# Kernel optimization log

Measured on AMD Instinct MI355X. Metric: run time of the kernel, lower is better.

The kernel has to match this reference:

```python
import jax, jax.numpy as jnp
import numpy as np

N_NODES = 50000
N_EDGES = 300000
D = 256


def setup_inputs() -> dict:
    key = jax.random.key(0)
    k1, k2, k3, k4, k5 = jax.random.split(key, 5)
    edge_feat = jax.random.normal(k1, (N_EDGES, D), dtype=jnp.float32)
    node_feat = jax.random.normal(k2, (N_NODES, D), dtype=jnp.float32)
    src_idx = jax.random.randint(k3, (N_EDGES,), 0, N_NODES, dtype=jnp.int32)
    tgt_idx = jax.random.randint(k4, (N_EDGES,), 0, N_NODES, dtype=jnp.int32)
    W = jax.random.normal(k5, (3 * D, D), dtype=jnp.float32) * (1.0 / np.sqrt(3 * D))
    b = jnp.zeros((D,), dtype=jnp.float32)
    return {"edge_feat": edge_feat, "node_feat": node_feat,
            "src_idx": src_idx, "tgt_idx": tgt_idx, "W": W, "b": b}


def reference(edge_feat, node_feat, src_idx, tgt_idx, W, b):
    # broadcast_node_to_edges: gather node states for SOURCE and TARGET tags
    src = jnp.take(node_feat, src_idx, axis=0)   # [E, D]
    tgt = jnp.take(node_feat, tgt_idx, axis=0)   # [E, D]
    # NextStateFromConcat: concat edge input + node inputs, then Dense+relu
    x = jnp.concatenate([edge_feat, src, tgt], axis=-1)  # [E, 3D]
    return jax.nn.relu(x @ W + b)                        # [E, D]
```

## Files before the change

### kernel.cpp

```cpp
#include <hip/hip_runtime.h>
#include <hip/hip_bf16.h>

typedef __attribute__((ext_vector_type(8))) short short8;
typedef __attribute__((ext_vector_type(4))) float floatx4;

#define D_DIM 256
#define K_DIM 768
#define BM 64
#define BK 32
#define PAD 40
#define NSTEP 24
#define BTILE 8192

__device__ __forceinline__ short f2bf(float x) {
    union { float f; unsigned u; } a; a.f = x;
    unsigned r = a.u + 0x7fffu + ((a.u >> 16) & 1u);
    return (short)(r >> 16);
}

__device__ __forceinline__ unsigned swz(unsigned r) {
    return r ^ (((r >> 7) & 7u) << 4);
}

__global__ __launch_bounds__(256) void wt_kernel(const float* __restrict__ W,
                                                 short* __restrict__ Wt2) {
    const int k = blockIdx.x;
    const int n = threadIdx.x;
    const int t = k >> 5, kk = k & 31;
    const unsigned r = (unsigned)n * 64u + (unsigned)kk * 2u;
    Wt2[(size_t)t * BTILE + (swz(r) >> 1)] = f2bf(W[(size_t)k * D_DIM + n]);
}

__global__ __launch_bounds__(256, 3) void edge_gemm(
    const float* __restrict__ edge, const float* __restrict__ node,
    const int* __restrict__ src, const int* __restrict__ tgt,
    const short* __restrict__ Wt2, const float* __restrict__ bias,
    float* __restrict__ out, int E)
{
    __shared__ __align__(16) short As[2][BM][PAD];
    __shared__ __align__(16) short Bs[2][BTILE];

    const int tid = threadIdx.x;
    const int m0 = blockIdx.x * BM;

    const int arow = tid >> 2;
    const int achk = (tid & 3) * 8;
    int rs = m0 + arow; if (rs >= E) rs = E - 1;
    const int si = src[rs], ti = tgt[rs];
    const float* a0 = edge + (size_t)rs * D_DIM + achk;
    const float* a1 = node + (size_t)si * D_DIM + achk;
    const float* a2 = node + (size_t)ti * D_DIM + achk;

    const int lane = tid & 63;
    const int wv = tid >> 6;
    const int fr = lane & 15;
    const int kq = (lane >> 4) * 8;

    const char* gb = (const char*)Wt2 + wv * 4096 + lane * 16;
    char* lb0 = (char*)&Bs[0][0] + wv * 4096;
    char* lb1 = (char*)&Bs[1][0] + wv * 4096;

    unsigned boff[4];
#pragma unroll
    for (int j = 0; j < 4; ++j) {
        unsigned col = (unsigned)(wv * 64 + j * 16 + fr);
        boff[j] = swz(col * 64u + (unsigned)(lane >> 4) * 16u);
    }

    floatx4 acc[4][4] = {};
    float4 pA0, pA1, qA0, qA1;

#define GLOADB(t, lb) { \
    const char* g_ = gb + (size_t)(t) * 16384; \
    __builtin_amdgcn_global_load_lds((const __attribute__((address_space(1))) unsigned*)(g_), \
        (__attribute__((address_space(3))) unsigned*)(lb), 16, 0, 0); \
    __builtin_amdgcn_global_load_lds((const __attribute__((address_space(1))) unsigned*)(g_ + 1024), \
        (__attribute__((address_space(3))) unsigned*)((lb) + 1024), 16, 0, 0); \
    __builtin_amdgcn_global_load_lds((const __attribute__((address_space(1))) unsigned*)(g_ + 2048), \
        (__attribute__((address_space(3))) unsigned*)((lb) + 2048), 16, 0, 0); \
    __builtin_amdgcn_global_load_lds((const __attribute__((address_space(1))) unsigned*)(g_ + 3072), \
        (__attribute__((address_space(3))) unsigned*)((lb) + 3072), 16, 0, 0); }

#define LOADA(d0, d1, t) { \
    const int sg_ = (t) >> 3; \
    const float* ab_ = sg_ == 0 ? a0 : (sg_ == 1 ? a1 : a2); \
    const float4* ap_ = (const float4*)(ab_ + ((t) & 7) * BK); \
    d0 = ap_[0]; d1 = ap_[1]; }

#define STOREA(b, s0, s1) { \
    union { short8 v; short s[8]; } u_; \
    u_.s[0] = f2bf(s0.x); u_.s[1] = f2bf(s0.y); u_.s[2] = f2bf(s0.z); u_.s[3] = f2bf(s0.w); \
    u_.s[4] = f2bf(s1.x); u_.s[5] = f2bf(s1.y); u_.s[6] = f2bf(s1.z); u_.s[7] = f2bf(s1.w); \
    *(short8*)&As[b][arow][achk] = u_.v; }

#define COMPUTE(b) { \
    const char* bb_ = (const char*)&Bs[b][0]; \
    short8 bfr0 = *(const short8*)(bb_ + boff[0]); \
    short8 bfr1 = *(const short8*)(bb_ + boff[1]); \
    short8 bfr2 = *(const short8*)(bb_ + boff[2]); \
    short8 bfr3 = *(const short8*)(bb_ + boff[3]); \
    _Pragma("unroll") \
    for (int i_ = 0; i_ < 4; ++i_) { \
        short8 afr = *(const short8*)&As[b][i_ * 16 + fr][kq]; \
        acc[i_][0] = __builtin_amdgcn_mfma_f32_16x16x32_bf16(afr, bfr0, acc[i_][0], 0, 0, 0); \
        acc[i_][1] = __builtin_amdgcn_mfma_f32_16x16x32_bf16(afr, bfr1, acc[i_][1], 0, 0, 0); \
        acc[i_][2] = __builtin_amdgcn_mfma_f32_16x16x32_bf16(afr, bfr2, acc[i_][2], 0, 0, 0); \
        acc[i_][3] = __builtin_amdgcn_mfma_f32_16x16x32_bf16(afr, bfr3, acc[i_][3], 0, 0, 0); \
    } }

    GLOADB(0, lb0);
    LOADA(qA0, qA1, 0);
    STOREA(0, qA0, qA1);
    LOADA(qA0, qA1, 1);
    __syncthreads();

#pragma unroll 1
    for (int t = 0; t < 22; t += 2) {
        GLOADB(t + 1, lb1);
        LOADA(pA0, pA1, t + 2);
        COMPUTE(0);
        STOREA(1, qA0, qA1);
        __syncthreads();
        GLOADB(t + 2, lb0);
        LOADA(qA0, qA1, t + 3);
        COMPUTE(1);
        STOREA(0, pA0, pA1);
        __syncthreads();
    }
    GLOADB(23, lb1);
    COMPUTE(0);
    STOREA(1, qA0, qA1);
    __syncthreads();
    COMPUTE(1);

#undef GLOADB
#undef LOADA
#undef STOREA
#undef COMPUTE

    float bv[4];
#pragma unroll
    for (int j = 0; j < 4; ++j) bv[j] = bias[wv * 64 + j * 16 + fr];
    const int rq = (lane >> 4) * 4;
#pragma unroll
    for (int i = 0; i < 4; ++i) {
        const int rbase = m0 + i * 16 + rq;
#pragma unroll
        for (int j = 0; j < 4; ++j) {
            const int c = wv * 64 + j * 16 + fr;
#pragma unroll
            for (int r = 0; r < 4; ++r) {
                const int rr = rbase + r;
                if (rr < E) {
                    float v = acc[i][j][r] + bv[j];
                    out[(size_t)rr * D_DIM + c] = v > 0.f ? v : 0.f;
                }
            }
        }
    }
}

extern "C" void kernel_launch(void* const* d_in, const int* in_sizes, int n_in,
                              void* d_out, int out_size, void* d_ws, size_t ws_size,
                              hipStream_t stream) {
    const float* edge = (const float*)d_in[0];
    const float* node = (const float*)d_in[1];
    const int*   srcI = (const int*)d_in[2];
    const int*   tgtI = (const int*)d_in[3];
    const float* W    = (const float*)d_in[4];
    const float* bias = (const float*)d_in[5];
    float* out = (float*)d_out;
    const int E = in_sizes[2];
    short* Wt2 = (short*)d_ws;

    wt_kernel<<<dim3(K_DIM), dim3(256), 0, stream>>>(W, Wt2);

    dim3 ggrid((E + BM - 1) / BM);
    edge_gemm<<<ggrid, dim3(256), 0, stream>>>(edge, node, srcI, tgtI, Wt2, bias, out, E);
}
```

Measured before the change: 661.0 us.

## Pre-convert node features to bf16 and gather them directly into LDS

Adds a pass that converts node features to bf16 in workspace. The GEMM then gathers the src/tgt rows with global_load_lds straight into swizzled LDS, with no register staging or per-edge conversion. The block tile doubles to 128 rows with 512 threads in a 2x4 wave layout so each weight tile is reused across more rows, and explicit waitcnt/barriers replace __syncthreads. In exchange, the extra conversion pass reads all node data once, node_cvt hardcodes the node count, and the fp32 path remains as a fallback when workspace is small.

```diff
diff --git a/kernel.cpp b/kernel.cpp
--- a/kernel.cpp
+++ b/kernel.cpp
@@ -4,13 +4,14 @@
 typedef __attribute__((ext_vector_type(8))) short short8;
 typedef __attribute__((ext_vector_type(4))) float floatx4;
 
+#define AS1G __attribute__((address_space(1)))
+#define AS3L __attribute__((address_space(3)))
+
 #define D_DIM 256
 #define K_DIM 768
-#define BM 64
-#define BK 32
-#define PAD 40
+#define BM 128
 #define NSTEP 24
-#define BTILE 8192
+#define N_NODES_C 50000
 
 __device__ __forceinline__ short f2bf(float x) {
     union { float f; unsigned u; } a; a.f = x;
@@ -18,9 +19,8 @@
     return (short)(r >> 16);
 }
 
-__device__ __forceinline__ unsigned swz(unsigned r) {
-    return r ^ (((r >> 7) & 7u) << 4);
-}
+__device__ __forceinline__ unsigned swzB(unsigned r) { return r ^ (((r >> 7) & 7u) << 4); }
+__device__ __forceinline__ unsigned swzA(unsigned r) { return r ^ (((r >> 7) & 3u) << 4); }
 
 __global__ __launch_bounds__(256) void wt_kernel(const float* __restrict__ W,
                                                  short* __restrict__ Wt2) {
@@ -28,126 +28,157 @@
     const int n = threadIdx.x;
     const int t = k >> 5, kk = k & 31;
     const unsigned r = (unsigned)n * 64u + (unsigned)kk * 2u;
-    Wt2[(size_t)t * BTILE + (swz(r) >> 1)] = f2bf(W[(size_t)k * D_DIM + n]);
-}
-
-__global__ __launch_bounds__(256, 3) void edge_gemm(
+    Wt2[(size_t)t * 8192 + (swzB(r) >> 1)] = f2bf(W[(size_t)k * D_DIM + n]);
+}
+
+__global__ __launch_bounds__(256) void node_cvt(const float* __restrict__ node,
+                                                short* __restrict__ nbf) {
+    const int i = blockIdx.x * 256 + threadIdx.x;
+    const float4* p = (const float4*)node + (size_t)i * 2;
+    float4 f0 = p[0], f1 = p[1];
+    union { short8 v; short s[8]; } u;
+    u.s[0] = f2bf(f0.x); u.s[1] = f2bf(f0.y); u.s[2] = f2bf(f0.z); u.s[3] = f2bf(f0.w);
+    u.s[4] = f2bf(f1.x); u.s[5] = f2bf(f1.y); u.s[6] = f2bf(f1.z); u.s[7] = f2bf(f1.w);
+    *((short8*)nbf + i) = u.v;
+}
+
+template<int NBF>
+__global__ __launch_bounds__(512, 4) void edge_gemm(
     const float* __restrict__ edge, const float* __restrict__ node,
     const int* __restrict__ src, const int* __restrict__ tgt,
-    const short* __restrict__ Wt2, const float* __restrict__ bias,
-    float* __restrict__ out, int E)
+    const short* __restrict__ Wt2, const short* __restrict__ nodebf,
+    const float* __restrict__ bias, float* __restrict__ out, int E)
 {
-    __shared__ __align__(16) short As[2][BM][PAD];
-    __shared__ __align__(16) short Bs[2][BTILE];
+    __shared__ __align__(16) short As[2][4096];
+    __shared__ __align__(16) short Bs[2][8192];
 
     const int tid = threadIdx.x;
     const int m0 = blockIdx.x * BM;
 
-    const int arow = tid >> 2;
-    const int achk = (tid & 3) * 8;
-    int rs = m0 + arow; if (rs >= E) rs = E - 1;
+    const int lane = tid & 63, wv = tid >> 6;
+    const int fr = lane & 15, u16 = (lane >> 4) * 16;
+    const int wm = (wv >> 2) * 64, wn = (wv & 3) * 64;
+
+    const int srow = tid >> 2;
+    const int q = (tid & 3) ^ ((srow >> 1) & 3);
+    const int qb = q * 16;
+    int rs = m0 + srow; if (rs >= E) rs = E - 1;
     const int si = src[rs], ti = tgt[rs];
-    const float* a0 = edge + (size_t)rs * D_DIM + achk;
-    const float* a1 = node + (size_t)si * D_DIM + achk;
-    const float* a2 = node + (size_t)ti * D_DIM + achk;
-
-    const int lane = tid & 63;
-    const int wv = tid >> 6;
-    const int fr = lane & 15;
-    const int kq = (lane >> 4) * 8;
-
-    const char* gb = (const char*)Wt2 + wv * 4096 + lane * 16;
-    char* lb0 = (char*)&Bs[0][0] + wv * 4096;
-    char* lb1 = (char*)&Bs[1][0] + wv * 4096;
-
-    unsigned boff[4];
-#pragma unroll
-    for (int j = 0; j < 4; ++j) {
-        unsigned col = (unsigned)(wv * 64 + j * 16 + fr);
-        boff[j] = swz(col * 64u + (unsigned)(lane >> 4) * 16u);
-    }
+    const char* eaf = (const char*)edge + (size_t)rs * 1024 + qb * 2;
+    const char* nb1; const char* nb2;
+    if constexpr (NBF) {
+        nb1 = (const char*)nodebf + (size_t)si * 512 + qb;
+        nb2 = (const char*)nodebf + (size_t)ti * 512 + qb;
+    } else {
+        nb1 = (const char*)node + (size_t)si * 1024 + qb * 2;
+        nb2 = (const char*)node + (size_t)ti * 1024 + qb * 2;
+    }
+
+    const char* gbB = (const char*)Wt2 + wv * 2048 + lane * 16;
+    char* lbA0 = (char*)As + wv * 1024;
+    char* lbA1 = (char*)As + 8192 + wv * 1024;
+    char* lbB0 = (char*)Bs + wv * 2048;
+    char* lbB1 = (char*)Bs + 16384 + wv * 2048;
+
+    unsigned aoff[4], boff[4];
+#pragma unroll
+    for (int i = 0; i < 4; ++i) { unsigned x = (unsigned)(wm + i * 16 + fr) * 64u + u16; aoff[i] = swzA(x); }
+#pragma unroll
+    for (int j = 0; j < 4; ++j) { unsigned x = (unsigned)(wn + j * 16 + fr) * 64u + u16; boff[j] = swzB(x); }
 
     floatx4 acc[4][4] = {};
     float4 pA0, pA1, qA0, qA1;
 
 #define GLOADB(t, lb) { \
-    const char* g_ = gb + (size_t)(t) * 16384; \
-    __builtin_amdgcn_global_load_lds((const __attribute__((address_space(1))) unsigned*)(g_), \
-        (__attribute__((address_space(3))) unsigned*)(lb), 16, 0, 0); \
-    __builtin_amdgcn_global_load_lds((const __attribute__((address_space(1))) unsigned*)(g_ + 1024), \
-        (__attribute__((address_space(3))) unsigned*)((lb) + 1024), 16, 0, 0); \
-    __builtin_amdgcn_global_load_lds((const __attribute__((address_space(1))) unsigned*)(g_ + 2048), \
-        (__attribute__((address_space(3))) unsigned*)((lb) + 2048), 16, 0, 0); \
-    __builtin_amdgcn_global_load_lds((const __attribute__((address_space(1))) unsigned*)(g_ + 3072), \
-        (__attribute__((address_space(3))) unsigned*)((lb) + 3072), 16, 0, 0); }
-
-#define LOADA(d0, d1, t) { \
-    const int sg_ = (t) >> 3; \
-    const float* ab_ = sg_ == 0 ? a0 : (sg_ == 1 ? a1 : a2); \
-    const float4* ap_ = (const float4*)(ab_ + ((t) & 7) * BK); \
-    d0 = ap_[0]; d1 = ap_[1]; }
-
-#define STOREA(b, s0, s1) { \
+    const char* g_ = gbB + (size_t)(t) * 16384; \
+    __builtin_amdgcn_global_load_lds((const AS1G unsigned*)(g_), (AS3L unsigned*)(lb), 16, 0, 0); \
+    __builtin_amdgcn_global_load_lds((const AS1G unsigned*)(g_ + 1024), (AS3L unsigned*)((lb) + 1024), 16, 0, 0); }
+
+#define GLOADA(ts, sp, lb) { \
+    __builtin_amdgcn_global_load_lds((const AS1G unsigned*)((sp) + (ts) * 64), (AS3L unsigned*)(lb), 16, 0, 0); }
+
+#define LOADA_S(d0, d1, t) { \
+    const char* b_ = (t) < 8 ? eaf : (((t) < 16) ? nb1 : nb2); \
+    b_ += ((t) & 7) * 128; \
+    d0 = *(const float4*)b_; d1 = *(const float4*)(b_ + 16); }
+
+#define STOREA(bi, s0, s1) { \
     union { short8 v; short s[8]; } u_; \
     u_.s[0] = f2bf(s0.x); u_.s[1] = f2bf(s0.y); u_.s[2] = f2bf(s0.z); u_.s[3] = f2bf(s0.w); \
     u_.s[4] = f2bf(s1.x); u_.s[5] = f2bf(s1.y); u_.s[6] = f2bf(s1.z); u_.s[7] = f2bf(s1.w); \
-    *(short8*)&As[b][arow][achk] = u_.v; }
-
-#define COMPUTE(b) { \
-    const char* bb_ = (const char*)&Bs[b][0]; \
+    *(short8*)((char*)As + (bi) * 8192 + tid * 16) = u_.v; }
+
+#define COMPUTE(bi) { \
+    const char* ab_ = (const char*)As + (bi) * 8192; \
+    const char* bb_ = (const char*)Bs + (bi) * 16384; \
     short8 bfr0 = *(const short8*)(bb_ + boff[0]); \
     short8 bfr1 = *(const short8*)(bb_ + boff[1]); \
     short8 bfr2 = *(const short8*)(bb_ + boff[2]); \
     short8 bfr3 = *(const short8*)(bb_ + boff[3]); \
     _Pragma("unroll") \
     for (int i_ = 0; i_ < 4; ++i_) { \
-        short8 afr = *(const short8*)&As[b][i_ * 16 + fr][kq]; \
+        short8 afr = *(const short8*)(ab_ + aoff[i_]); \
         acc[i_][0] = __builtin_amdgcn_mfma_f32_16x16x32_bf16(afr, bfr0, acc[i_][0], 0, 0, 0); \
         acc[i_][1] = __builtin_amdgcn_mfma_f32_16x16x32_bf16(afr, bfr1, acc[i_][1], 0, 0, 0); \
         acc[i_][2] = __builtin_amdgcn_mfma_f32_16x16x32_bf16(afr, bfr2, acc[i_][2], 0, 0, 0); \
         acc[i_][3] = __builtin_amdgcn_mfma_f32_16x16x32_bf16(afr, bfr3, acc[i_][3], 0, 0, 0); \
     } }
 
-    GLOADB(0, lb0);
-    LOADA(qA0, qA1, 0);
+#define WAIT2 { asm volatile("s_waitcnt vmcnt(2) lgkmcnt(0)" ::: "memory"); __builtin_amdgcn_sched_barrier(0); }
+#define WAIT0 { asm volatile("s_waitcnt vmcnt(0) lgkmcnt(0)" ::: "memory"); __builtin_amdgcn_sched_barrier(0); }
+#define BARX  { __builtin_amdgcn_s_barrier(); __builtin_amdgcn_sched_barrier(0); }
+
+    LOADA_S(qA0, qA1, 0);
+    GLOADB(0, lbB0);
     STOREA(0, qA0, qA1);
-    LOADA(qA0, qA1, 1);
-    __syncthreads();
-
+    LOADA_S(qA0, qA1, 1);
+
+    if constexpr (NBF) {
 #pragma unroll 1
-    for (int t = 0; t < 22; t += 2) {
-        GLOADB(t + 1, lb1);
-        LOADA(pA0, pA1, t + 2);
-        COMPUTE(0);
-        STOREA(1, qA0, qA1);
-        __syncthreads();
-        GLOADB(t + 2, lb0);
-        LOADA(qA0, qA1, t + 3);
-        COMPUTE(1);
-        STOREA(0, pA0, pA1);
-        __syncthreads();
-    }
-    GLOADB(23, lb1);
-    COMPUTE(0);
-    STOREA(1, qA0, qA1);
-    __syncthreads();
-    COMPUTE(1);
+        for (int t = 0; t < 6; t += 2) {
+            WAIT2; BARX; GLOADB(t + 1, lbB1); LOADA_S(pA0, pA1, t + 2); COMPUTE(0); STOREA(1, qA0, qA1);
+            WAIT2; BARX; GLOADB(t + 2, lbB0); LOADA_S(qA0, qA1, t + 3); COMPUTE(1); STOREA(0, pA0, pA1);
+        }
+        WAIT2; BARX; GLOADB(7, lbB1); COMPUTE(0); STOREA(1, qA0, qA1);
+        WAIT0; BARX; GLOADB(8, lbB0); GLOADA(0, nb1, lbA0); COMPUTE(1);
+#pragma unroll 1
+        for (int t = 8; t < 22; t += 2) {
+            const char* s1 = ((t + 1) < 16) ? nb1 : nb2;
+            WAIT0; BARX; GLOADB(t + 1, lbB1); GLOADA((t + 1) & 7, s1, lbA1); COMPUTE(0);
+            const char* s2 = ((t + 2) < 16) ? nb1 : nb2;
+            WAIT0; BARX; GLOADB(t + 2, lbB0); GLOADA((t + 2) & 7, s2, lbA0); COMPUTE(1);
+        }
+        WAIT0; BARX; GLOADB(23, lbB1); GLOADA(7, nb2, lbA1); COMPUTE(0);
+        WAIT0; BARX; COMPUTE(1);
+    } else {
+#pragma unroll 1
+        for (int t = 0; t < 22; t += 2) {
+            WAIT2; BARX; GLOADB(t + 1, lbB1); LOADA_S(pA0, pA1, t + 2); COMPUTE(0); STOREA(1, qA0, qA1);
+            WAIT2; BARX; GLOADB(t + 2, lbB0); LOADA_S(qA0, qA1, t + 3); COMPUTE(1); STOREA(0, pA0, pA1);
+        }
+        WAIT2; BARX; GLOADB(23, lbB1); COMPUTE(0); STOREA(1, qA0, qA1);
+        WAIT0; BARX; COMPUTE(1);
+    }
 
 #undef GLOADB
-#undef LOADA
+#undef GLOADA
+#undef LOADA_S
 #undef STOREA
 #undef COMPUTE
+#undef WAIT2
+#undef WAIT0
+#undef BARX
 
     float bv[4];
 #pragma unroll
-    for (int j = 0; j < 4; ++j) bv[j] = bias[wv * 64 + j * 16 + fr];
+    for (int j = 0; j < 4; ++j) bv[j] = bias[wn + j * 16 + fr];
     const int rq = (lane >> 4) * 4;
 #pragma unroll
     for (int i = 0; i < 4; ++i) {
-        const int rbase = m0 + i * 16 + rq;
+        const int rbase = m0 + wm + i * 16 + rq;
 #pragma unroll
         for (int j = 0; j < 4; ++j) {
-            const int c = wv * 64 + j * 16 + fr;
+            const int c = wn + j * 16 + fr;
 #pragma unroll
             for (int r = 0; r < 4; ++r) {
                 const int rr = rbase + r;
@@ -171,10 +202,18 @@
     const float* bias = (const float*)d_in[5];
     float* out = (float*)d_out;
     const int E = in_sizes[2];
+
     short* Wt2 = (short*)d_ws;
+    short* nodebf = (short*)((char*)d_ws + 393216);
+    const size_t WS_NEED = 393216u + (size_t)N_NODES_C * D_DIM * 2u;
 
     wt_kernel<<<dim3(K_DIM), dim3(256), 0, stream>>>(W, Wt2);
 
     dim3 ggrid((E + BM - 1) / BM);
-    edge_gemm<<<ggrid, dim3(256), 0, stream>>>(edge, node, srcI, tgtI, Wt2, bias, out, E);
-}
+    if (ws_size >= WS_NEED) {
+        node_cvt<<<dim3(N_NODES_C * D_DIM / 8 / 256), dim3(256), 0, stream>>>(node, nodebf);
+        edge_gemm<1><<<ggrid, dim3(512), 0, stream>>>(edge, node, srcI, tgtI, Wt2, nodebf, bias, out, E);
+    } else {
+        edge_gemm<0><<<ggrid, dim3(512), 0, stream>>>(edge, node, srcI, tgtI, Wt2, nodebf, bias, out, E);
+    }
+}
```

Result: no change. 655.8 us (-0.8%).
